# Kernel tuning notes

Measured on AMD Instinct MI355X. Metric: run time of the kernel, lower is better.

The kernel has to match this reference:

```python
import jax, jax.numpy as jnp
import numpy as np

N_NODES = 10000
N_EDGES = 160000
MUL = 16            # multiplicity: emb_dim=64, max_l=1 -> irreps 16x0e + 16x1o
EMB = 64
NUM_BASIS = 10
MAX_RADIUS = 4.5
HIDDEN = 64
N_PATHS = 4         # (0e,0e->0e), (0e,1o->1o), (1o,0e->1o), (1o,1o->0e)
W_NUMEL = N_PATHS * MUL * MUL  # 1024


def setup_inputs() -> dict:
    key = jax.random.key(0)
    ks = jax.random.split(key, 6)
    x = jax.random.normal(ks[0], (N_NODES, EMB), jnp.float32)
    src = jax.random.randint(ks[1], (N_EDGES,), 0, N_NODES)
    dst = jax.random.randint(ks[2], (N_EDGES,), 0, N_NODES)
    edge_vec = jax.random.normal(ks[3], (N_EDGES, 3), jnp.float32)
    mlp_w1 = jax.random.normal(ks[4], (NUM_BASIS, HIDDEN), jnp.float32)
    mlp_w2 = jax.random.normal(ks[5], (HIDDEN, W_NUMEL), jnp.float32)
    return {"x": x, "edge_vec": edge_vec, "mlp_w1": mlp_w1,
            "mlp_w2": mlp_w2, "src": src, "dst": dst}


def _sus(t):
    # e3nn smooth bump helper: exp(-1/t) for t>0 else 0
    return jnp.where(t > 0, jnp.exp(-1.0 / jnp.where(t > 0, t, 1.0)), 0.0)


def _radial_embedding(r):
    # soft_one_hot_linspace(basis='smooth_finite', cutoff=True), then *sqrt(num_basis)
    values = jnp.linspace(0.0, MAX_RADIUS, NUM_BASIS + 2)[1:-1]
    step = MAX_RADIUS / (NUM_BASIS + 1)
    diff = (r[:, None] - values) / step                     # [E, NUM_BASIS]
    basis = 1.14136 * jnp.exp(2.0) * _sus(diff + 1.0) * _sus(1.0 - diff)
    return basis * (NUM_BASIS ** 0.5)


def _forward(x, edge_vec, mlp_w1, mlp_w2, src, dst):
    E = edge_vec.shape[0]
    N = x.shape[0]
    r = jnp.linalg.norm(edge_vec, axis=1)                   # [E]
    # spherical harmonics, lmax=1, normalize=True, 'component' norm: Y0=1, Y1=sqrt(3)*n
    y1 = jnp.sqrt(3.0) * edge_vec / r[:, None]              # [E, 3]

    # radial MLP (e3nn FullyConnectedNet: W~N(0,1), x@W/sqrt(fan_in), relu scaled by sqrt(2))
    emb = _radial_embedding(r)                              # [E, 10]
    h = jnp.sqrt(2.0) * jax.nn.relu(emb @ (mlp_w1 / NUM_BASIS ** 0.5))
    w = h @ (mlp_w2 / HIDDEN ** 0.5)                        # [E, 1024]
    w = w.reshape(E, N_PATHS, MUL, MUL)                     # paths in e3nn order A,B,C,D

    xs = x[src]                                             # gather [E, 64]
    x0 = xs[:, :MUL]                                        # [E, 16] 0e scalars
    x1 = xs[:, MUL:].reshape(E, MUL, 3)                     # [E, 16, 3] 1o vectors

    # Fully connected TP normalization ('component', path_norm 'element'):
    # out0 fan = 2*MUL -> alpha 1/(2*MUL); out1 alpha 3/(2*MUL) with w3j 1/sqrt(3)
    c = 1.0 / jnp.sqrt(2.0 * MUL)
    inv_sqrt3 = 1.0 / jnp.sqrt(3.0)
    wA, wB, wC, wD = w[:, 0], w[:, 1], w[:, 2], w[:, 3]
    # 0e outputs: 0e*0e->0e and 1o*1o->0e (dot product, w3j = I/sqrt(3))
    out0 = c * (jnp.einsum('euw,eu->ew', wA, x0)
                + inv_sqrt3 * jnp.einsum('euw,eum,em->ew', wD, x1, y1))
    # 1o outputs: 0e*1o->1o and 1o*0e->1o (w3j = I/sqrt(3), Y0 = 1)
    out1 = c * (jnp.einsum('euw,eu,em->ewm', wB, x0, y1)
                + jnp.einsum('euw,eum->ewm', wC, x1))
    summand = jnp.concatenate([out0, out1.reshape(E, MUL * 3)], axis=1)  # [E, 64]

    out = jax.ops.segment_sum(summand, dst, num_segments=N)             # [N, 64]
    return out * (N / E)


def reference(x, edge_vec, mlp_w1, mlp_w2, src, dst):
    return _forward(x, edge_vec, mlp_w1, mlp_w2, src, dst)
```

## Files before the change

kernel.cpp:

```cpp
#include <hip/hip_runtime.h>
#include <hip/hip_bf16.h>


typedef __attribute__((ext_vector_type(8))) short bf16x8;
typedef __attribute__((ext_vector_type(4))) float f32x4;

#define NN 10000
#define NE 160000

__device__ __forceinline__ float sus_f(float t) { return t > 0.0f ? __expf(-1.0f / t) : 0.0f; }
__device__ __forceinline__ unsigned int f2bf(float f) {
    unsigned int u = __float_as_uint(f);
    u += 0x7FFFu + ((u >> 16) & 1u);
    return u >> 16;
}
__device__ __forceinline__ float bf2f(unsigned short v) { return __uint_as_float(((unsigned int)v) << 16); }

#define GL16(g, l) __builtin_amdgcn_global_load_lds( \
    (const __attribute__((address_space(1))) void*)(g), \
    (__attribute__((address_space(3))) void*)(l), 16, 0, 0)

__device__ __forceinline__ void stage_lds(const void* g, void* l, int bytes, int wv, int lane) {
    const char* gc = (const char*)g;
    char* lc = (char*)l;
    const int units = bytes >> 4;
    for (int u0 = wv << 6; u0 < units; u0 += 512) {
        if (u0 + lane < units) GL16(gc + (((long)(u0 + lane)) << 4), lc + (u0 << 4));
    }
}

__global__ void hist_k(const int* __restrict__ dst, int* __restrict__ hist,
                       const float* __restrict__ w2, char* __restrict__ w2bf) {
    if (blockIdx.x < 625) {
        const int e = blockIdx.x * 256 + threadIdx.x;
        if (e < NE) atomicAdd(&hist[dst[e]], 1);
    } else {
        const int idx = (blockIdx.x - 625) * 256 + threadIdx.x;
        const int j = idx >> 10, R = idx & 1023;
        unsigned int pk[4];
        #pragma unroll
        for (int p = 0; p < 4; ++p) {
            const unsigned int lo = f2bf(w2[(size_t)(8 * j + 2 * p) * 1024 + R]);
            const unsigned int hi = f2bf(w2[(size_t)(8 * j + 2 * p + 1) * 1024 + R]);
            pk[p] = lo | (hi << 16);
        }
        uint4 v; v.x = pk[0]; v.y = pk[1]; v.z = pk[2]; v.w = pk[3];
        *(uint4*)(w2bf + R * 128 + ((j ^ (R & 7)) << 4)) = v;
    }
}

__global__ __launch_bounds__(1024) void scan_k(const int* __restrict__ hist,
                                               int* __restrict__ offsets) {
    __shared__ int hl[NN];
    __shared__ int wsum[16];
    const int tid = threadIdx.x;
    for (int i = tid; i < NN; i += 1024) hl[i] = hist[i];
    __syncthreads();
    const int base = tid * 10;
    int loc[10]; int s = 0;
    #pragma unroll
    for (int i = 0; i < 10; ++i) { loc[i] = s; const int b = base + i; s += (b < NN) ? hl[b] : 0; }
    int v = s;
    const int lane = tid & 63, wv = tid >> 6;
    #pragma unroll
    for (int d = 1; d < 64; d <<= 1) { int t2 = __shfl_up(v, d); if (lane >= d) v += t2; }
    if (lane == 63) wsum[wv] = v;
    __syncthreads();
    if (tid < 64) {
        int w = (tid < 16) ? wsum[tid] : 0;
        #pragma unroll
        for (int d = 1; d < 16; d <<= 1) { int t2 = __shfl_up(w, d); if (tid >= d) w += t2; }
        if (tid < 16) wsum[tid] = w;
    }
    __syncthreads();
    const int wexc = (wv == 0) ? 0 : wsum[wv - 1];
    const int texc = wexc + v - s;
    #pragma unroll
    for (int i = 0; i < 10; ++i) { const int b = base + i; if (b < NN) offsets[b] = texc + loc[i]; }
    if (tid == 1023) offsets[NN] = texc + s;
}

// ... 12 lines not shown
__global__ __launch_bounds__(256, 4) void prep_k(
    const float* __restrict__ x, const float* __restrict__ edge_vec,
    const float* __restrict__ w1, const int* __restrict__ src,
    const int* __restrict__ perm,
    char* __restrict__ h_bf, char* __restrict__ X0g, char* __restrict__ Zg,
    char* __restrict__ X1g, float* __restrict__ Y1g)
{
    __shared__ float embl[128][10];
    __shared__ float y1l[128][4];
    __shared__ int srcl[128];
    __shared__ float w1l[640];
    const int tid = threadIdx.x;
    const long e0 = (long)blockIdx.x * 128;

    for (int i = tid; i < 640; i += 256) w1l[i] = w1[i];
    if (tid < 128) {
        const int e = tid;
        const int eid = perm[e0 + e];
        const float vx = edge_vec[eid * 3 + 0];
        const float vy = edge_vec[eid * 3 + 1];
        const float vz = edge_vec[eid * 3 + 2];
        const float r = sqrtf(vx * vx + vy * vy + vz * vz);
        const float sc = 1.7320508075688772f / r;
        y1l[e][0] = vx * sc; y1l[e][1] = vy * sc; y1l[e][2] = vz * sc; y1l[e][3] = 0.f;
        *(float4*)&Y1g[(e0 + e) * 4] = make_float4(vx * sc, vy * sc, vz * sc, 0.f);
        srcl[e] = src[eid];
        const float C0 = 1.14136f * __expf(2.0f) * 3.1622776601683795f;
        #pragma unroll
        for (int i = 0; i < 10; ++i) {
            const float diff = r * (11.0f / 4.5f) - (float)(i + 1);
            embl[e][i] = C0 * sus_f(diff + 1.0f) * sus_f(1.0f - diff);
        }
    }
    __syncthreads();
    for (int idx = tid; idx < 1024; idx += 256) {
        const int e = idx >> 3, j = idx & 7;
        float acc[8];
        #pragma unroll
        for (int jj = 0; jj < 8; ++jj) acc[jj] = 0.0f;
        #pragma unroll
        for (int i = 0; i < 10; ++i) {
            const float ei = embl[e][i];
            #pragma unroll
            for (int jj = 0; jj < 8; ++jj) acc[jj] += ei * w1l[i * 64 + j * 8 + jj];
        }
        unsigned int pk[4];
        #pragma unroll
        for (int p = 0; p < 4; ++p) {
            const unsigned int lo = f2bf(fmaxf(acc[2 * p],     0.0f) * 0.4472135954999579f);
            const unsigned int hi = f2bf(fmaxf(acc[2 * p + 1], 0.0f) * 0.4472135954999579f);
            pk[p] = lo | (hi << 16);
        }
        uint4 v; v.x = pk[0]; v.y = pk[1]; v.z = pk[2]; v.w = pk[3];
        *(uint4*)(h_bf + (e0 + e) * 128 + ((j ^ (e & 7)) << 4)) = v;
    }
    for (int idx = tid; idx < 1024; idx += 256) {
        const int e = idx >> 3, p = idx & 7;
        const int s = srcl[e];
        const float2 ab = *(const float2*)&x[(size_t)s * 64 + 2 * p];
        *(unsigned int*)(X0g + (e0 + e) * 36 + p * 4) = f2bf(ab.x) | (f2bf(ab.y) << 16);
    }
    for (int idx = tid; idx < 1024; idx += 256) {
        const int e = idx >> 3, p = idx & 7;
        const int s = srcl[e];
        const float* xp = x + (size_t)s * 64 + 16 + 6 * p;
        const float z0 = xp[0] * y1l[e][0] + xp[1] * y1l[e][1] + xp[2] * y1l[e][2];
        const float z1 = xp[3] * y1l[e][0] + xp[4] * y1l[e][1] + xp[5] * y1l[e][2];
        *(unsigned int*)(Zg + (e0 + e) * 36 + p * 4) = f2bf(z0) | (f2bf(z1) << 16);
    }
    for (int idx = tid; idx < 128 * 12; idx += 256) {
        const int e = idx / 12, qd = idx - e * 12;
        const int s = srcl[e];
        const float4 v = *(const float4*)&x[(size_t)s * 64 + 16 + 4 * qd];
        *(float4*)(X1g + (e0 + e) * 208 + qd * 16) = v;
    }
}

#define BUF_SZ 48128

__global__ __launch_bounds__(512, 2) void se3_edge2(
    const char* __restrict__ w2bf, const char* __restrict__ h_bf,
    const char* __restrict__ X0g, const char* __restrict__ Zg,
    const char* __restrict__ X1g, const float* __restrict__ Y1g,
    const int* __restrict__ dsts, float* __restrict__ out)
{
    __shared__ __align__(16) char w2lds[65536];
    __shared__ __align__(16) char bufs[2][BUF_SZ];
    __shared__ int segst[2][66];
    __shared__ int nseg[2];

    const int tid = threadIdx.x, lane = tid & 63, wv = tid >> 6;
    const int lm = lane & 15, q = lane >> 4;
    const int bx = blockIdx.x;
    const int pair = (bx & 1) ^ ((bx >> 8) & 1);
    const int tb = bx >> 1;
    const int s0 = (q ^ (lm & 7)) << 4;
    const int s1 = s0 ^ 64;
    const int erow = wv << 4;

    const char* w2p0 = w2lds;
    const char* w2p1 = w2lds + 32768;
    {
        const int pa = pair ? 1 : 0, pb = pair ? 2 : 3;
        stage_lds(w2bf + pa * 32768, w2lds, 32768, wv, lane);
        stage_lds(w2bf + pb * 32768, w2lds + 32768, 32768, wv, lane);
        const long e0 = (long)tb * 5 * 128;
        stage_lds(h_bf + e0 * 128, bufs[0], 16384, wv, lane);
        stage_lds(X0g + e0 * 36, bufs[0] + 16384, 4608, wv, lane);
        if (pair) stage_lds(X1g + e0 * 208, bufs[0] + 20992, 26624, wv, lane);
        else      stage_lds(Zg  + e0 * 36,  bufs[0] + 20992, 4608,  wv, lane);
        stage_lds((const char*)(dsts + e0), bufs[0] + 47616, 512, wv, lane);
    }
    __syncthreads();

    const float S = 0.17677669529663687f * 0.125f * 0.0625f;

    for (int tt = 0; tt < 5; ++tt) {
        char* buf = bufs[tt & 1];
        const long gt = (long)tb * 5 + tt;
        const long e0 = gt * 128;
        if (tt < 4) {
            char* nb = bufs[(tt & 1) ^ 1];
            const long ne0 = e0 + 128;
            stage_lds(h_bf + ne0 * 128, nb, 16384, wv, lane);
            stage_lds(X0g + ne0 * 36, nb + 16384, 4608, wv, lane);
            if (pair) stage_lds(X1g + ne0 * 208, nb + 20992, 26624, wv, lane);
            else      stage_lds(Zg  + ne0 * 36,  nb + 20992, 4608,  wv, lane);
            stage_lds((const char*)(dsts + ne0), nb + 47616, 512, wv, lane);
        }
        const char* hl = buf;
        const int arow = erow + lm;
        const bf16x8 a0 = *(const bf16x8*)(hl + arow * 128 + s0);
        const bf16x8 a1 = *(const bf16x8*)(hl + arow * 128 + s1);
        const unsigned short* X0l = (const unsigned short*)(buf + 16384);
        const int* dstl = (const int*)(buf + 47616);

        float ac0[4] = {0,0,0,0}, ac1[4] = {0,0,0,0}, ac2[4] = {0,0,0,0}, ac3[4] = {0,0,0,0};

        if (pair == 0) {
            const unsigned short* Zl = (const unsigned short*)(buf + 20992);
            #pragma unroll 4
            for (int t = 0; t < 16; ++t) {
                const int rowb = (t * 16 + lm) << 7;
                const bf16x8 b00 = *(const bf16x8*)(w2p0 + rowb + s0);
                const bf16x8 b01 = *(const bf16x8*)(w2p0 + rowb + s1);
                const bf16x8 b10 = *(const bf16x8*)(w2p1 + rowb + s0);
                const bf16x8 b11 = *(const bf16x8*)(w2p1 + rowb + s1);
                f32x4 wA = {0.f,0.f,0.f,0.f};
                wA = __builtin_amdgcn_mfma_f32_16x16x32_bf16(a0, b00, wA, 0,0,0);
                wA = __builtin_amdgcn_mfma_f32_16x16x32_bf16(a1, b01, wA, 0,0,0);
                f32x4 wD = {0.f,0.f,0.f,0.f};
                wD = __builtin_amdgcn_mfma_f32_16x16x32_bf16(a0, b10, wD, 0,0,0);
                wD = __builtin_amdgcn_mfma_f32_16x16x32_bf16(a1, b11, wD, 0,0,0);
                #pragma unroll
                for (int r = 0; r < 4; ++r) {
                    const int el = erow + 4 * q + r;
                    ac0[r] += wA[r] * bf2f(X0l[el * 18 + t]);
                    ac1[r] += wD[r] * bf2f(Zl[el * 18 + t]);
                }
            }
            float* summ32 = (float*)buf;
            #pragma unroll
            for (int r = 0; r < 4; ++r) {
                const int el = erow + 4 * q + r;
                summ32[el * 17 + lm] = S * (ac0[r] + 0.5773502691896258f * ac1[r]);
            }
        } else {
            const float* X1l = (const float*)(buf + 20992);
            #pragma unroll 4
            for (int t = 0; t < 16; ++t) {
                const int rowb = (t * 16 + lm) << 7;
                const bf16x8 b00 = *(const bf16x8*)(w2p0 + rowb + s0);
                const bf16x8 b01 = *(const bf16x8*)(w2p0 + rowb + s1);
                const bf16x8 b10 = *(const bf16x8*)(w2p1 + rowb + s0);
                const bf16x8 b11 = *(const bf16x8*)(w2p1 + rowb + s1);
                f32x4 wB = {0.f,0.f,0.f,0.f};
                wB = __builtin_amdgcn_mfma_f32_16x16x32_bf16(a0, b00, wB, 0,0,0);
                wB = __builtin_amdgcn_mfma_f32_16x16x32_bf16(a1, b01, wB, 0,0,0);
                f32x4 wC = {0.f,0.f,0.f,0.f};
                wC = __builtin_amdgcn_mfma_f32_16x16x32_bf16(a0, b10, wC, 0,0,0);
                wC = __builtin_amdgcn_mfma_f32_16x16x32_bf16(a1, b11, wC, 0,0,0);
                #pragma unroll
                for (int r = 0; r < 4; ++r) {
                    const int el = erow + 4 * q + r;
                    ac0[r] += wB[r] * bf2f(X0l[el * 18 + t]);
                    ac1[r] += wC[r] * X1l[el * 52 + 3 * t + 0];
                    ac2[r] += wC[r] * X1l[el * 52 + 3 * t + 1];
                    ac3[r] += wC[r] * X1l[el * 52 + 3 * t + 2];
                }
            }
            unsigned short* summ16 = (unsigned short*)buf;
            #pragma unroll
            for (int r = 0; r < 4; ++r) {
                const int el = erow + 4 * q + r;
                const float4 y = *(const float4*)&Y1g[(e0 + el) * 4];
                const float b = S * ac0[r];
                summ16[el * 49 + 3 * lm + 0] = (unsigned short)f2bf(b * y.x + S * ac1[r]);
                summ16[el * 49 + 3 * lm + 1] = (unsigned short)f2bf(b * y.y + S * ac2[r]);
                summ16[el * 49 + 3 * lm + 2] = (unsigned short)f2bf(b * y.z + S * ac3[r]);
            }
        }
        if (wv < 2) {
            const int base = wv << 6;
            const int d = dstl[base + lane];
            const bool flag = (lane == 0) || (d != dstl[base + lane - 1]);
            const unsigned long long m = __ballot(flag);
            const int sid = (lane == 0) ? 0 : __popcll(m & ((1ull << lane) - 1ull));
            if (flag) segst[wv][sid] = base + lane;
            if (lane == 63) { const int ns = __popcll(m); nseg[wv] = ns; segst[wv][ns] = base + 64; }
        }
        __syncthreads();
        const int nsa = nseg[0], nsb = nseg[1];
        if (pair == 0) {
            const float* summ32 = (const float*)buf;
            const int total = (nsa + nsb) * 16;
            for (int i = tid; i < total; i += 512) {
                const int sg = i >> 4, c = i & 15;
                const int hh = sg >= nsa;
                const int sl = hh ? sg - nsa : sg;
                const int eb = segst[hh][sl], ee = segst[hh][sl + 1];
                float sum = 0.f;
                for (int e = eb; e < ee; ++e) sum += summ32[e * 17 + c];
                atomicAdd(&out[(size_t)dstl[eb] * 64 + c], sum);
            }
        } else {
            const unsigned short* summ16 = (const unsigned short*)buf;
            const int total = (nsa + nsb) * 48;
            for (int i = tid; i < total; i += 512) {
                const int sg = i / 48, c = i - sg * 48;
                const int hh = sg >= nsa;
                const int sl = hh ? sg - nsa : sg;
                const int eb = segst[hh][sl], ee = segst[hh][sl + 1];
                float sum = 0.f;
                for (int e = eb; e < ee; ++e) sum += bf2f(summ16[e * 49 + c]);
                atomicAdd(&out[(size_t)dstl[eb] * 64 + 16 + c], sum);
            }
        }
        __syncthreads();
    }
}

#define FBT 64
template<int PATH>
__device__ __forceinline__ void fb_body(
    const float* __restrict__ x, const float* __restrict__ edge_vec,
    const float* __restrict__ w1, const float* __restrict__ w2,
    const int* __restrict__ src, const int* __restrict__ perm,
    const int* __restrict__ dsts, float* __restrict__ out,
    unsigned short (*w2t)[72], float* arena, float (*y1l)[4],
    int* dstl, int* srcl, int* segstart, int* nseg_s)
{
    constexpr int NC    = (PATH == 0 || PATH == 3) ? 16 : 48;
    constexpr int CBASE = (PATH == 0 || PATH == 3) ? 0 : 16;
    const int tid = threadIdx.x;
    float* embl = arena;
    unsigned short* hl = (unsigned short*)(arena + 640);
    float* feats = arena + 2944;
    float* summ  = arena;
    {
        const float* col = w2 + PATH * 256 + tid;
        #pragma unroll
        for (int k = 0; k < 64; k += 2) {
            const unsigned int lo = f2bf(col[(size_t)k * 1024]);
            const unsigned int hi = f2bf(col[(size_t)(k + 1) * 1024]);
            *(unsigned int*)&w2t[tid][k] = lo | (hi << 16);
        }
    }
    const int lane = tid & 63, wv = tid >> 6, lm = lane & 15, q = lane >> 4;
    const int erow = wv * 16;
    const float C0 = 1.14136f * __expf(2.0f) * 3.1622776601683795f;
    const float S  = 0.17677669529663687f * 0.125f * 0.0625f;
    for (int it = 0; it < 2; ++it) {
        const int e0 = (blockIdx.x * 2 + it) * FBT;
        __syncthreads();
        for (int idx = tid; idx < FBT * 10; idx += 256) {
            const int e = idx / 10, i = idx - e * 10;
            const int eid = perm[e0 + e];
            const float vx = edge_vec[eid * 3 + 0], vy = edge_vec[eid * 3 + 1], vz = edge_vec[eid * 3 + 2];
            const float r = sqrtf(vx * vx + vy * vy + vz * vz);
            const float diff = r * (11.0f / 4.5f) - (float)(i + 1);
            embl[e * 10 + i] = C0 * sus_f(diff + 1.0f) * sus_f(1.0f - diff);
            if (i == 0) {
                const float sc = 1.7320508075688772f / r;
                y1l[e][0] = vx * sc; y1l[e][1] = vy * sc; y1l[e][2] = vz * sc;
                dstl[e] = dsts[e0 + e];
                srcl[e] = src[eid];
            }
        }
        __syncthreads();
// ... 91 lines not shown
            const int eb = segstart[s], ee = segstart[s + 1];
            float sum = 0.0f;
            for (int e = eb; e < ee; ++e) sum += summ[e * NC + c];
            atomicAdd(&out[(size_t)dstl[eb] * 64 + CBASE + c], sum);
        }
    }
}

__global__ __launch_bounds__(256, 2) void fb_edge(
    const float* __restrict__ x, const float* __restrict__ edge_vec,
    const float* __restrict__ w1, const float* __restrict__ w2,
    const int* __restrict__ src, const int* __restrict__ perm,
    const int* __restrict__ dsts, float* __restrict__ out)
{
    __shared__ unsigned short w2t[256][72];
    __shared__ float arena[6016];
    __shared__ float y1l[FBT][4];
    __shared__ int dstl[FBT];
    __shared__ int srcl[FBT];
    __shared__ int segstart[FBT + 1];
    __shared__ int nseg_s;
    switch (blockIdx.y) {
        case 0:  fb_body<0>(x, edge_vec, w1, w2, src, perm, dsts, out, w2t, arena, y1l, dstl, srcl, segstart, &nseg_s); break;
        case 1:  fb_body<1>(x, edge_vec, w1, w2, src, perm, dsts, out, w2t, arena, y1l, dstl, srcl, segstart, &nseg_s); break;
        case 2:  fb_body<2>(x, edge_vec, w1, w2, src, perm, dsts, out, w2t, arena, y1l, dstl, srcl, segstart, &nseg_s); break;
        default: fb_body<3>(x, edge_vec, w1, w2, src, perm, dsts, out, w2t, arena, y1l, dstl, srcl, segstart, &nseg_s); break;
    }
}

extern "C" void kernel_launch(void* const* d_in, const int* in_sizes, int n_in,
                              void* d_out, int out_size, void* d_ws, size_t ws_size,
                              hipStream_t stream) {
    const float* x        = (const float*)d_in[0];
    const float* edge_vec = (const float*)d_in[1];
    const float* w1       = (const float*)d_in[2];
    const float* w2       = (const float*)d_in[3];
    const int*   src      = (const int*)d_in[4];
    const int*   dst      = (const int*)d_in[5];
    float* out = (float*)d_out;

    char* ws = (char*)d_ws;
    size_t off = 0;
    auto alloc = [&](size_t n) -> char* {
        off = (off + 255) & ~(size_t)255;
        char* p = ws + off; off += n; return p;
    };
    int* hist    = (int*)alloc(40000);
    int* cursor  = (int*)alloc(40000);
    int* offsets = (int*)alloc(40004);
    int* perm    = (int*)alloc(640000);
    int* dsts    = (int*)alloc(640000);
    char* w2bf   = alloc(131072);
    char* h_bf   = alloc((size_t)NE * 128);
    char* X0g    = alloc((size_t)NE * 36);
    char* Zg     = alloc((size_t)NE * 36);
    float* Y1g   = (float*)alloc((size_t)NE * 16);
    char* X1g    = alloc((size_t)NE * 208);
    const bool big = (off <= ws_size);

    hipMemsetAsync(d_out, 0, (size_t)out_size * sizeof(float), stream);
    hipMemsetAsync(d_ws, 0, 81408, stream);

    if (big) {
        hipLaunchKernelGGL(hist_k, dim3(657), dim3(256), 0, stream, dst, hist, w2, w2bf);
        hipLaunchKernelGGL(scan_k, dim3(1), dim3(1024), 0, stream, hist, offsets);
        hipLaunchKernelGGL(scatter_k, dim3(625), dim3(256), 0, stream, dst, offsets, cursor, perm, dsts);
        hipLaunchKernelGGL(prep_k, dim3(1250), dim3(256), 0, stream,
                           x, edge_vec, w1, src, perm, h_bf, X0g, Zg, X1g, Y1g);
        hipLaunchKernelGGL(se3_edge2, dim3(500), dim3(512), 0, stream,
                           w2bf, h_bf, X0g, Zg, X1g, Y1g, dsts, out);
    } else {
        hipLaunchKernelGGL(hist_k, dim3(625), dim3(256), 0, stream, dst, hist, w2, w2bf);
        hipLaunchKernelGGL(scan_k, dim3(1), dim3(1024), 0, stream, hist, offsets);
        hipLaunchKernelGGL(scatter_k, dim3(625), dim3(256), 0, stream, dst, offsets, cursor, perm, dsts);
        hipLaunchKernelGGL(fb_edge, dim3(1250, 4), dim3(256), 0, stream,
                           x, edge_vec, w1, w2, src, perm, dsts, out);
    }
}
```

Measured before the change: 126.8 us.

## Split edge kernel into per-path kernels with smaller LDS footprint

Replaces the single paired-path edge kernel, which kept two w2 slices in LDS, with two kernels (A/D and B/C). Each block stages only one 32KB w2 slice, so more blocks can share a CU. The A operand h is now read directly from global instead of being staged, X1 is packed as bf16 in a transposed per-tile layout, and the per-edge features are held in registers. The cost is reading h_bf twice per edge pair, an extra launch, and a further bf16 rounding of X1.

```diff
diff --git a/kernel.cpp b/kernel.cpp
--- a/kernel.cpp
+++ b/kernel.cpp
@@ -3,6 +3,7 @@
 
 
 typedef __attribute__((ext_vector_type(8))) short bf16x8;
+typedef __attribute__((ext_vector_type(8))) unsigned short u16x8;
 typedef __attribute__((ext_vector_type(4))) float f32x4;
 
 #define NN 10000
@@ -15,18 +16,19 @@
     return u >> 16;
 }
 __device__ __forceinline__ float bf2f(unsigned short v) { return __uint_as_float(((unsigned int)v) << 16); }
+__device__ __forceinline__ float bflo(unsigned int v) { return __uint_as_float(v << 16); }
+__device__ __forceinline__ float bfhi(unsigned int v) { return __uint_as_float(v & 0xFFFF0000u); }
+__device__ __forceinline__ float bfe(u16x8 v, int i) { return __uint_as_float(((unsigned int)v[i]) << 16); }
 
 #define GL16(g, l) __builtin_amdgcn_global_load_lds( \
     (const __attribute__((address_space(1))) void*)(g), \
     (__attribute__((address_space(3))) void*)(l), 16, 0, 0)
 
-__device__ __forceinline__ void stage_lds(const void* g, void* l, int bytes, int wv, int lane) {
+__device__ __forceinline__ void stageN(const void* g, void* l, int bytes, int tid, int nthr) {
     const char* gc = (const char*)g;
     char* lc = (char*)l;
     const int units = bytes >> 4;
-    for (int u0 = wv << 6; u0 < units; u0 += 512) {
-        if (u0 + lane < units) GL16(gc + (((long)(u0 + lane)) << 4), lc + (u0 << 4));
-    }
+    for (int u = tid; u < units; u += nthr) GL16(gc + ((long)u << 4), lc + (u << 4));
 }
 
 __global__ void hist_k(const int* __restrict__ dst, int* __restrict__ hist,
@@ -145,13 +147,13 @@
             pk[p] = lo | (hi << 16);
         }
         uint4 v; v.x = pk[0]; v.y = pk[1]; v.z = pk[2]; v.w = pk[3];
-        *(uint4*)(h_bf + (e0 + e) * 128 + ((j ^ (e & 7)) << 4)) = v;
+        *(uint4*)(h_bf + (e0 + e) * 128 + (j << 4)) = v;
     }
     for (int idx = tid; idx < 1024; idx += 256) {
         const int e = idx >> 3, p = idx & 7;
         const int s = srcl[e];
         const float2 ab = *(const float2*)&x[(size_t)s * 64 + 2 * p];
-        *(unsigned int*)(X0g + (e0 + e) * 36 + p * 4) = f2bf(ab.x) | (f2bf(ab.y) << 16);
+        *(unsigned int*)(X0g + (e0 + e) * 32 + p * 4) = f2bf(ab.x) | (f2bf(ab.y) << 16);
     }
     for (int idx = tid; idx < 1024; idx += 256) {
         const int e = idx >> 3, p = idx & 7;
@@ -159,139 +161,83 @@
         const float* xp = x + (size_t)s * 64 + 16 + 6 * p;
         const float z0 = xp[0] * y1l[e][0] + xp[1] * y1l[e][1] + xp[2] * y1l[e][2];
         const float z1 = xp[3] * y1l[e][0] + xp[4] * y1l[e][1] + xp[5] * y1l[e][2];
-        *(unsigned int*)(Zg + (e0 + e) * 36 + p * 4) = f2bf(z0) | (f2bf(z1) << 16);
-    }
-    for (int idx = tid; idx < 128 * 12; idx += 256) {
-        const int e = idx / 12, qd = idx - e * 12;
+        *(unsigned int*)(Zg + (e0 + e) * 32 + p * 4) = f2bf(z0) | (f2bf(z1) << 16);
+    }
+    for (int idx = tid; idx < 2048; idx += 256) {
+        const int e = idx >> 4, u = idx & 15;
         const int s = srcl[e];
-        const float4 v = *(const float4*)&x[(size_t)s * 64 + 16 + 4 * qd];
-        *(float4*)(X1g + (e0 + e) * 208 + qd * 16) = v;
-    }
-}
-
-#define BUF_SZ 48128
-
-__global__ __launch_bounds__(512, 2) void se3_edge2(
+        const float* xp = x + (size_t)s * 64 + 16 + 3 * u;
+        uint2 v;
+        v.x = f2bf(xp[0]) | (f2bf(xp[1]) << 16);
+        v.y = f2bf(xp[2]);
+        *(uint2*)(X1g + (size_t)blockIdx.x * 16384 + ((u << 7) + e) * 8) = v;
+    }
+}
+
+__global__ __launch_bounds__(512, 6) void edge_ad(
     const char* __restrict__ w2bf, const char* __restrict__ h_bf,
     const char* __restrict__ X0g, const char* __restrict__ Zg,
-    const char* __restrict__ X1g, const float* __restrict__ Y1g,
     const int* __restrict__ dsts, float* __restrict__ out)
 {
-    __shared__ __align__(16) char w2lds[65536];
-    __shared__ __align__(16) char bufs[2][BUF_SZ];
+    __shared__ __align__(16) char w2lds[32768];
+    __shared__ __align__(16) char feats[2][4608];
+    __shared__ float summ[16 * 132];
     __shared__ int segst[2][66];
     __shared__ int nseg[2];
 
     const int tid = threadIdx.x, lane = tid & 63, wv = tid >> 6;
-    const int lm = lane & 15, q = lane >> 4;
-    const int bx = blockIdx.x;
-    const int pair = (bx & 1) ^ ((bx >> 8) & 1);
-    const int tb = bx >> 1;
-    const int s0 = (q ^ (lm & 7)) << 4;
-    const int s1 = s0 ^ 64;
-    const int erow = wv << 4;
-
-    const char* w2p0 = w2lds;
-    const char* w2p1 = w2lds + 32768;
+    const int lm = lane & 15, q = lane >> 4, erow = wv << 4;
+    const int isD = blockIdx.y;
+    const char* featg = isD ? Zg : X0g;
+    const int tb = blockIdx.x;
+    const int s0 = (q ^ (lm & 7)) << 4, s1 = s0 ^ 64;
+    const float S = 0.17677669529663687f * 0.125f * 0.0625f;
+    const float scl = isD ? S * 0.5773502691896258f : S;
+
+    stageN(w2bf + (isD ? 3 : 0) * 32768, w2lds, 32768, tid, 512);
     {
-        const int pa = pair ? 1 : 0, pb = pair ? 2 : 3;
-        stage_lds(w2bf + pa * 32768, w2lds, 32768, wv, lane);
-        stage_lds(w2bf + pb * 32768, w2lds + 32768, 32768, wv, lane);
         const long e0 = (long)tb * 5 * 128;
-        stage_lds(h_bf + e0 * 128, bufs[0], 16384, wv, lane);
-        stage_lds(X0g + e0 * 36, bufs[0] + 16384, 4608, wv, lane);
-        if (pair) stage_lds(X1g + e0 * 208, bufs[0] + 20992, 26624, wv, lane);
-        else      stage_lds(Zg  + e0 * 36,  bufs[0] + 20992, 4608,  wv, lane);
-        stage_lds((const char*)(dsts + e0), bufs[0] + 47616, 512, wv, lane);
+        stageN(featg + e0 * 32, feats[0], 4096, tid, 512);
+        stageN((const char*)(dsts + e0), feats[0] + 4096, 512, tid, 512);
     }
     __syncthreads();
 
-    const float S = 0.17677669529663687f * 0.125f * 0.0625f;
-
     for (int tt = 0; tt < 5; ++tt) {
-        char* buf = bufs[tt & 1];
-        const long gt = (long)tb * 5 + tt;
-        const long e0 = gt * 128;
+        char* fb = feats[tt & 1];
+        const long e0 = ((long)tb * 5 + tt) * 128;
         if (tt < 4) {
-            char* nb = bufs[(tt & 1) ^ 1];
-            const long ne0 = e0 + 128;
-            stage_lds(h_bf + ne0 * 128, nb, 16384, wv, lane);
-            stage_lds(X0g + ne0 * 36, nb + 16384, 4608, wv, lane);
-            if (pair) stage_lds(X1g + ne0 * 208, nb + 20992, 26624, wv, lane);
-            else      stage_lds(Zg  + ne0 * 36,  nb + 20992, 4608,  wv, lane);
-            stage_lds((const char*)(dsts + ne0), nb + 47616, 512, wv, lane);
-        }
-        const char* hl = buf;
+            char* nb = feats[(tt & 1) ^ 1];
+            stageN(featg + (e0 + 128) * 32, nb, 4096, tid, 512);
+            stageN((const char*)(dsts + e0 + 128), nb + 4096, 512, tid, 512);
+        }
         const int arow = erow + lm;
-        const bf16x8 a0 = *(const bf16x8*)(hl + arow * 128 + s0);
-        const bf16x8 a1 = *(const bf16x8*)(hl + arow * 128 + s1);
-        const unsigned short* X0l = (const unsigned short*)(buf + 16384);
-        const int* dstl = (const int*)(buf + 47616);
-
-        float ac0[4] = {0,0,0,0}, ac1[4] = {0,0,0,0}, ac2[4] = {0,0,0,0}, ac3[4] = {0,0,0,0};
-
-        if (pair == 0) {
-            const unsigned short* Zl = (const unsigned short*)(buf + 20992);
-            #pragma unroll 4
-            for (int t = 0; t < 16; ++t) {
-                const int rowb = (t * 16 + lm) << 7;
-                const bf16x8 b00 = *(const bf16x8*)(w2p0 + rowb + s0);
-                const bf16x8 b01 = *(const bf16x8*)(w2p0 + rowb + s1);
-                const bf16x8 b10 = *(const bf16x8*)(w2p1 + rowb + s0);
-                const bf16x8 b11 = *(const bf16x8*)(w2p1 + rowb + s1);
-                f32x4 wA = {0.f,0.f,0.f,0.f};
-                wA = __builtin_amdgcn_mfma_f32_16x16x32_bf16(a0, b00, wA, 0,0,0);
-                wA = __builtin_amdgcn_mfma_f32_16x16x32_bf16(a1, b01, wA, 0,0,0);
-                f32x4 wD = {0.f,0.f,0.f,0.f};
-                wD = __builtin_amdgcn_mfma_f32_16x16x32_bf16(a0, b10, wD, 0,0,0);
-                wD = __builtin_amdgcn_mfma_f32_16x16x32_bf16(a1, b11, wD, 0,0,0);
-                #pragma unroll
-                for (int r = 0; r < 4; ++r) {
-                    const int el = erow + 4 * q + r;
-                    ac0[r] += wA[r] * bf2f(X0l[el * 18 + t]);
-                    ac1[r] += wD[r] * bf2f(Zl[el * 18 + t]);
-                }
-            }
-            float* summ32 = (float*)buf;
-            #pragma unroll
-            for (int r = 0; r < 4; ++r) {
-                const int el = erow + 4 * q + r;
-                summ32[el * 17 + lm] = S * (ac0[r] + 0.5773502691896258f * ac1[r]);
-            }
-        } else {
-            const float* X1l = (const float*)(buf + 20992);
-            #pragma unroll 4
-            for (int t = 0; t < 16; ++t) {
-                const int rowb = (t * 16 + lm) << 7;
-                const bf16x8 b00 = *(const bf16x8*)(w2p0 + rowb + s0);
-                const bf16x8 b01 = *(const bf16x8*)(w2p0 + rowb + s1);
-                const bf16x8 b10 = *(const bf16x8*)(w2p1 + rowb + s0);
-                const bf16x8 b11 = *(const bf16x8*)(w2p1 + rowb + s1);
-                f32x4 wB = {0.f,0.f,0.f,0.f};
-                wB = __builtin_amdgcn_mfma_f32_16x16x32_bf16(a0, b00, wB, 0,0,0);
-                wB = __builtin_amdgcn_mfma_f32_16x16x32_bf16(a1, b01, wB, 0,0,0);
-                f32x4 wC = {0.f,0.f,0.f,0.f};
-                wC = __builtin_amdgcn_mfma_f32_16x16x32_bf16(a0, b10, wC, 0,0,0);
-                wC = __builtin_amdgcn_mfma_f32_16x16x32_bf16(a1, b11, wC, 0,0,0);
-                #pragma unroll
-                for (int r = 0; r < 4; ++r) {
-                    const int el = erow + 4 * q + r;
-                    ac0[r] += wB[r] * bf2f(X0l[el * 18 + t]);
-                    ac1[r] += wC[r] * X1l[el * 52 + 3 * t + 0];
-                    ac2[r] += wC[r] * X1l[el * 52 + 3 * t + 1];
-                    ac3[r] += wC[r] * X1l[el * 52 + 3 * t + 2];
-                }
-            }
-            unsigned short* summ16 = (unsigned short*)buf;
-            #pragma unroll
-            for (int r = 0; r < 4; ++r) {
-                const int el = erow + 4 * q + r;
-                const float4 y = *(const float4*)&Y1g[(e0 + el) * 4];
-                const float b = S * ac0[r];
-                summ16[el * 49 + 3 * lm + 0] = (unsigned short)f2bf(b * y.x + S * ac1[r]);
-                summ16[el * 49 + 3 * lm + 1] = (unsigned short)f2bf(b * y.y + S * ac2[r]);
-                summ16[el * 49 + 3 * lm + 2] = (unsigned short)f2bf(b * y.z + S * ac3[r]);
-            }
+        const bf16x8 a0 = *(const bf16x8*)(h_bf + (e0 + arow) * 128 + q * 16);
+        const bf16x8 a1 = *(const bf16x8*)(h_bf + (e0 + arow) * 128 + 64 + q * 16);
+        u16x8 flo[4], fhi[4];
+        #pragma unroll
+        for (int r = 0; r < 4; ++r) {
+            const int el = erow + 4 * q + r;
+            flo[r] = *(const u16x8*)(fb + el * 32);
+            fhi[r] = *(const u16x8*)(fb + el * 32 + 16);
+        }
+        float ac[4] = {0.f, 0.f, 0.f, 0.f};
+        #pragma unroll
+        for (int t = 0; t < 16; ++t) {
+            const int rowb = (t * 16 + lm) << 7;
+            const bf16x8 b0 = *(const bf16x8*)(w2lds + rowb + s0);
+            const bf16x8 b1 = *(const bf16x8*)(w2lds + rowb + s1);
+            f32x4 w = {0.f, 0.f, 0.f, 0.f};
+            w = __builtin_amdgcn_mfma_f32_16x16x32_bf16(a0, b0, w, 0, 0, 0);
+            w = __builtin_amdgcn_mfma_f32_16x16x32_bf16(a1, b1, w, 0, 0, 0);
+            #pragma unroll
+            for (int r = 0; r < 4; ++r)
+                ac[r] += w[r] * (t < 8 ? bfe(flo[r], t) : bfe(fhi[r], t - 8));
+        }
+        const int* dstl = (const int*)(fb + 4096);
+        #pragma unroll
+        for (int r = 0; r < 4; ++r) {
+            const int el = erow + 4 * q + r;
+            summ[lm * 132 + el] = scl * ac[r];
         }
         if (wv < 2) {
             const int base = wv << 6;
@@ -304,30 +250,143 @@
         }
         __syncthreads();
         const int nsa = nseg[0], nsb = nseg[1];
-        if (pair == 0) {
-            const float* summ32 = (const float*)buf;
-            const int total = (nsa + nsb) * 16;
-            for (int i = tid; i < total; i += 512) {
-                const int sg = i >> 4, c = i & 15;
-                const int hh = sg >= nsa;
-                const int sl = hh ? sg - nsa : sg;
-                const int eb = segst[hh][sl], ee = segst[hh][sl + 1];
-                float sum = 0.f;
-                for (int e = eb; e < ee; ++e) sum += summ32[e * 17 + c];
-                atomicAdd(&out[(size_t)dstl[eb] * 64 + c], sum);
-            }
+        const int total = (nsa + nsb) << 4;
+        for (int i = tid; i < total; i += 512) {
+            const int sg = i >> 4, c = i & 15;
+            const int hh = (sg >= nsa) ? 1 : 0;
+            const int sl = hh ? sg - nsa : sg;
+            const int eb = segst[hh][sl], ee = segst[hh][sl + 1];
+            float s = 0.f;
+            for (int e = eb; e < ee; ++e) s += summ[c * 132 + e];
+            atomicAdd(&out[(size_t)dstl[eb] * 64 + c], s);
+        }
+        __syncthreads();
+    }
+}
+
+#define FEATSZ 16896
+
+__global__ __launch_bounds__(512, 4) void edge_bc(
+    const char* __restrict__ w2bf, const char* __restrict__ h_bf,
+    const char* __restrict__ X0g, const char* __restrict__ X1g,
+    const float* __restrict__ Y1g, const int* __restrict__ dsts,
+    float* __restrict__ out)
+{
+    __shared__ __align__(16) char w2lds[32768];
+    __shared__ __align__(16) char feats[2][FEATSZ];
+    __shared__ unsigned short summ[48 * 132];
+    __shared__ int segst[2][66];
+    __shared__ int nseg[2];
+
+    const int tid = threadIdx.x, lane = tid & 63, wv = tid >> 6;
+    const int lm = lane & 15, q = lane >> 4, erow = wv << 4;
+    const int isC = blockIdx.y;
+    const int tb = blockIdx.x;
+    const int s0 = (q ^ (lm & 7)) << 4, s1 = s0 ^ 64;
+    const int dstoff = isC ? 16384 : 6144;
+    const float S = 0.17677669529663687f * 0.125f * 0.0625f;
+
+    auto stage_tile = [&](char* nb, long e0) {
+        if (isC) {
+            stageN(X1g + (e0 >> 7) * 16384, nb, 16384, tid, 512);
         } else {
-            const unsigned short* summ16 = (const unsigned short*)buf;
-            const int total = (nsa + nsb) * 48;
-            for (int i = tid; i < total; i += 512) {
-                const int sg = i / 48, c = i - sg * 48;
-                const int hh = sg >= nsa;
-                const int sl = hh ? sg - nsa : sg;
-                const int eb = segst[hh][sl], ee = segst[hh][sl + 1];
-                float sum = 0.f;
-                for (int e = eb; e < ee; ++e) sum += bf2f(summ16[e * 49 + c]);
-                atomicAdd(&out[(size_t)dstl[eb] * 64 + 16 + c], sum);
-            }
+            stageN(X0g + e0 * 32, nb, 4096, tid, 512);
+            stageN((const char*)(Y1g + e0 * 4), nb + 4096, 2048, tid, 512);
+        }
+        stageN((const char*)(dsts + e0), nb + dstoff, 512, tid, 512);
+    };
+
+    stageN(w2bf + (isC ? 2 : 1) * 32768, w2lds, 32768, tid, 512);
+    stage_tile(feats[0], (long)tb * 5 * 128);
+    __syncthreads();
+
+    for (int tt = 0; tt < 5; ++tt) {
+        char* fb = feats[tt & 1];
+        const long e0 = ((long)tb * 5 + tt) * 128;
+        if (tt < 4) stage_tile(feats[(tt & 1) ^ 1], e0 + 128);
+
+        const int arow = erow + lm;
+        const bf16x8 a0 = *(const bf16x8*)(h_bf + (e0 + arow) * 128 + q * 16);
+        const bf16x8 a1 = *(const bf16x8*)(h_bf + (e0 + arow) * 128 + 64 + q * 16);
+
+        if (isC) {
+            float ac1[4] = {0,0,0,0}, ac2[4] = {0,0,0,0}, ac3[4] = {0,0,0,0};
+            #pragma unroll
+            for (int t = 0; t < 16; ++t) {
+                const int rowb = (t * 16 + lm) << 7;
+                const bf16x8 b0 = *(const bf16x8*)(w2lds + rowb + s0);
+                const bf16x8 b1 = *(const bf16x8*)(w2lds + rowb + s1);
+                f32x4 w = {0.f, 0.f, 0.f, 0.f};
+                w = __builtin_amdgcn_mfma_f32_16x16x32_bf16(a0, b0, w, 0, 0, 0);
+                w = __builtin_amdgcn_mfma_f32_16x16x32_bf16(a1, b1, w, 0, 0, 0);
+                #pragma unroll
+                for (int r = 0; r < 4; ++r) {
+                    const int el = erow + 4 * q + r;
+                    const uint2 xv = *(const uint2*)(fb + ((t << 7) + el) * 8);
+                    ac1[r] += w[r] * bflo(xv.x);
+                    ac2[r] += w[r] * bfhi(xv.x);
+                    ac3[r] += w[r] * bflo(xv.y);
+                }
+            }
+            #pragma unroll
+            for (int r = 0; r < 4; ++r) {
+                const int el = erow + 4 * q + r;
+                summ[(3 * lm + 0) * 132 + el] = (unsigned short)f2bf(S * ac1[r]);
+                summ[(3 * lm + 1) * 132 + el] = (unsigned short)f2bf(S * ac2[r]);
+                summ[(3 * lm + 2) * 132 + el] = (unsigned short)f2bf(S * ac3[r]);
+            }
+        } else {
+            u16x8 flo[4], fhi[4];
+            #pragma unroll
+            for (int r = 0; r < 4; ++r) {
+                const int el = erow + 4 * q + r;
+                flo[r] = *(const u16x8*)(fb + el * 32);
+                fhi[r] = *(const u16x8*)(fb + el * 32 + 16);
+            }
+            float ac[4] = {0.f, 0.f, 0.f, 0.f};
+            #pragma unroll
+            for (int t = 0; t < 16; ++t) {
+                const int rowb = (t * 16 + lm) << 7;
+                const bf16x8 b0 = *(const bf16x8*)(w2lds + rowb + s0);
+                const bf16x8 b1 = *(const bf16x8*)(w2lds + rowb + s1);
+                f32x4 w = {0.f, 0.f, 0.f, 0.f};
+                w = __builtin_amdgcn_mfma_f32_16x16x32_bf16(a0, b0, w, 0, 0, 0);
+                w = __builtin_amdgcn_mfma_f32_16x16x32_bf16(a1, b1, w, 0, 0, 0);
+                #pragma unroll
+                for (int r = 0; r < 4; ++r)
+                    ac[r] += w[r] * (t < 8 ? bfe(flo[r], t) : bfe(fhi[r], t - 8));
+            }
+            #pragma unroll
+            for (int r = 0; r < 4; ++r) {
+                const int el = erow + 4 * q + r;
+                const float4 y = *(const float4*)(fb + 4096 + el * 16);
+                const float b = S * ac[r];
+                summ[(3 * lm + 0) * 132 + el] = (unsigned short)f2bf(b * y.x);
+                summ[(3 * lm + 1) * 132 + el] = (unsigned short)f2bf(b * y.y);
+                summ[(3 * lm + 2) * 132 + el] = (unsigned short)f2bf(b * y.z);
+            }
+        }
+        const int* dstl = (const int*)(fb + dstoff);
+        if (wv < 2) {
+            const int base = wv << 6;
+            const int d = dstl[base + lane];
+            const bool flag = (lane == 0) || (d != dstl[base + lane - 1]);
+            const unsigned long long m = __ballot(flag);
+            const int sid = (lane == 0) ? 0 : __popcll(m & ((1ull << lane) - 1ull));
+            if (flag) segst[wv][sid] = base + lane;
+            if (lane == 63) { const int ns = __popcll(m); nseg[wv] = ns; segst[wv][ns] = base + 64; }
+        }
+        __syncthreads();
+        const int nsa = nseg[0], nsb = nseg[1];
+        const int total = (nsa + nsb) * 48;
+        for (int i = tid; i < total; i += 512) {
+            const int sg = i / 48, c = i - sg * 48;
+            const int hh = (sg >= nsa) ? 1 : 0;
+            const int sl = hh ? sg - nsa : sg;
+            const int eb = segst[hh][sl], ee = segst[hh][sl + 1];
+            float s = 0.f;
+            for (int e = eb; e < ee; ++e) s += bf2f(summ[c * 132 + e]);
+            atomicAdd(&out[(size_t)dstl[eb] * 64 + 16 + c], s);
         }
         __syncthreads();
     }
@@ -525,10 +584,10 @@
     int* dsts    = (int*)alloc(640000);
     char* w2bf   = alloc(131072);
     char* h_bf   = alloc((size_t)NE * 128);
-    char* X0g    = alloc((size_t)NE * 36);
-    char* Zg     = alloc((size_t)NE * 36);
+    char* X0g    = alloc((size_t)NE * 32);
+    char* Zg     = alloc((size_t)NE * 32);
+    char* X1g    = alloc((size_t)NE * 128);
     float* Y1g   = (float*)alloc((size_t)NE * 16);
-    char* X1g    = alloc((size_t)NE * 208);
     const bool big = (off <= ws_size);
 
     hipMemsetAsync(d_out, 0, (size_t)out_size * sizeof(float), stream);
@@ -540,8 +599,10 @@
         hipLaunchKernelGGL(scatter_k, dim3(625), dim3(256), 0, stream, dst, offsets, cursor, perm, dsts);
         hipLaunchKernelGGL(prep_k, dim3(1250), dim3(256), 0, stream,
                            x, edge_vec, w1, src, perm, h_bf, X0g, Zg, X1g, Y1g);
-        hipLaunchKernelGGL(se3_edge2, dim3(500), dim3(512), 0, stream,
-                           w2bf, h_bf, X0g, Zg, X1g, Y1g, dsts, out);
+        hipLaunchKernelGGL(edge_bc, dim3(250, 2), dim3(512), 0, stream,
+                           w2bf, h_bf, X0g, X1g, Y1g, dsts, out);
+        hipLaunchKernelGGL(edge_ad, dim3(250, 2), dim3(512), 0, stream,
+                           w2bf, h_bf, X0g, Zg, dsts, out);
     } else {
         hipLaunchKernelGGL(hist_k, dim3(625), dim3(256), 0, stream, dst, hist, w2, w2bf);
         hipLaunchKernelGGL(scan_k, dim3(1), dim3(1024), 0, stream, hist, offsets);
```

Measured after the change: 153.8 us. 1.21x slower.

## Compact per-edge staging layouts, load hidden activations directly, separate summand buffer

Applied to the files above, without the earlier changes.

Prep now stores X0/Z at 32 bytes per edge instead of 36, and stores X1 as bf16 in a component-major tile layout. Y1 is staged into LDS rather than read from global memory. The edge kernel reads the MLP hidden activations straight from global memory into MFMA operands instead of staging them through LDS. It also preloads the X0/Z values into registers, writes summands to a dedicated transposed LDS buffer, and launches a 2D grid by path pair. The aim is to cut global and LDS traffic and the per-buffer LDS footprint. In exchange X1 loses precision from fp32 to bf16, and the unstaged h loads may add latency.

```diff
diff --git a/kernel.cpp b/kernel.cpp
--- a/kernel.cpp
+++ b/kernel.cpp
@@ -3,6 +3,7 @@
 
 
 typedef __attribute__((ext_vector_type(8))) short bf16x8;
+typedef __attribute__((ext_vector_type(8))) unsigned short u16x8;
 typedef __attribute__((ext_vector_type(4))) float f32x4;
 
 #define NN 10000
@@ -15,18 +16,19 @@
     return u >> 16;
 }
 __device__ __forceinline__ float bf2f(unsigned short v) { return __uint_as_float(((unsigned int)v) << 16); }
+__device__ __forceinline__ float bflo(unsigned int v) { return __uint_as_float(v << 16); }
+__device__ __forceinline__ float bfhi(unsigned int v) { return __uint_as_float(v & 0xFFFF0000u); }
+__device__ __forceinline__ float bfe(u16x8 v, int i) { return __uint_as_float(((unsigned int)v[i]) << 16); }
 
 #define GL16(g, l) __builtin_amdgcn_global_load_lds( \
     (const __attribute__((address_space(1))) void*)(g), \
     (__attribute__((address_space(3))) void*)(l), 16, 0, 0)
 
-__device__ __forceinline__ void stage_lds(const void* g, void* l, int bytes, int wv, int lane) {
+__device__ __forceinline__ void stageN(const void* g, void* l, int bytes, int tid, int nthr) {
     const char* gc = (const char*)g;
     char* lc = (char*)l;
     const int units = bytes >> 4;
-    for (int u0 = wv << 6; u0 < units; u0 += 512) {
-        if (u0 + lane < units) GL16(gc + (((long)(u0 + lane)) << 4), lc + (u0 << 4));
-    }
+    for (int u = tid; u < units; u += nthr) GL16(gc + ((long)u << 4), lc + (u << 4));
 }
 
 __global__ void hist_k(const int* __restrict__ dst, int* __restrict__ hist,
@@ -145,13 +147,13 @@
             pk[p] = lo | (hi << 16);
         }
         uint4 v; v.x = pk[0]; v.y = pk[1]; v.z = pk[2]; v.w = pk[3];
-        *(uint4*)(h_bf + (e0 + e) * 128 + ((j ^ (e & 7)) << 4)) = v;
+        *(uint4*)(h_bf + (e0 + e) * 128 + (j << 4)) = v;
     }
     for (int idx = tid; idx < 1024; idx += 256) {
         const int e = idx >> 3, p = idx & 7;
         const int s = srcl[e];
         const float2 ab = *(const float2*)&x[(size_t)s * 64 + 2 * p];
-        *(unsigned int*)(X0g + (e0 + e) * 36 + p * 4) = f2bf(ab.x) | (f2bf(ab.y) << 16);
+        *(unsigned int*)(X0g + (e0 + e) * 32 + p * 4) = f2bf(ab.x) | (f2bf(ab.y) << 16);
     }
     for (int idx = tid; idx < 1024; idx += 256) {
         const int e = idx >> 3, p = idx & 7;
@@ -159,140 +161,150 @@
         const float* xp = x + (size_t)s * 64 + 16 + 6 * p;
         const float z0 = xp[0] * y1l[e][0] + xp[1] * y1l[e][1] + xp[2] * y1l[e][2];
         const float z1 = xp[3] * y1l[e][0] + xp[4] * y1l[e][1] + xp[5] * y1l[e][2];
-        *(unsigned int*)(Zg + (e0 + e) * 36 + p * 4) = f2bf(z0) | (f2bf(z1) << 16);
-    }
-    for (int idx = tid; idx < 128 * 12; idx += 256) {
-        const int e = idx / 12, qd = idx - e * 12;
+        *(unsigned int*)(Zg + (e0 + e) * 32 + p * 4) = f2bf(z0) | (f2bf(z1) << 16);
+    }
+    for (int idx = tid; idx < 2048; idx += 256) {
+        const int e = idx >> 4, u = idx & 15;
         const int s = srcl[e];
-        const float4 v = *(const float4*)&x[(size_t)s * 64 + 16 + 4 * qd];
-        *(float4*)(X1g + (e0 + e) * 208 + qd * 16) = v;
-    }
-}
-
-#define BUF_SZ 48128
-
-__global__ __launch_bounds__(512, 2) void se3_edge2(
+        const float* xp = x + (size_t)s * 64 + 16 + 3 * u;
+        uint2 v;
+        v.x = f2bf(xp[0]) | (f2bf(xp[1]) << 16);
+        v.y = f2bf(xp[2]);
+        *(uint2*)(X1g + (size_t)blockIdx.x * 16384 + ((u << 7) + e) * 8) = v;
+    }
+}
+
+#define DSTOFF 22784
+#define EBUF 23296
+
+__global__ __launch_bounds__(512, 2) void se3_edge(
     const char* __restrict__ w2bf, const char* __restrict__ h_bf,
     const char* __restrict__ X0g, const char* __restrict__ Zg,
     const char* __restrict__ X1g, const float* __restrict__ Y1g,
     const int* __restrict__ dsts, float* __restrict__ out)
 {
     __shared__ __align__(16) char w2lds[65536];
-    __shared__ __align__(16) char bufs[2][BUF_SZ];
+    __shared__ __align__(16) char bufs[2][EBUF];
+    __shared__ __align__(16) char summb[12672];
     __shared__ int segst[2][66];
     __shared__ int nseg[2];
 
     const int tid = threadIdx.x, lane = tid & 63, wv = tid >> 6;
-    const int lm = lane & 15, q = lane >> 4;
-    const int bx = blockIdx.x;
-    const int pair = (bx & 1) ^ ((bx >> 8) & 1);
-    const int tb = bx >> 1;
-    const int s0 = (q ^ (lm & 7)) << 4;
-    const int s1 = s0 ^ 64;
-    const int erow = wv << 4;
+    const int lm = lane & 15, q = lane >> 4, erow = wv << 4;
+    const int pair = blockIdx.y;
+    const int tb = blockIdx.x;
+    const int s0 = (q ^ (lm & 7)) << 4, s1 = s0 ^ 64;
+    const float S = 0.17677669529663687f * 0.125f * 0.0625f;
+
+    auto stage_tile = [&](char* nb, long e0) {
+        stageN(X0g + e0 * 32, nb, 4096, tid, 512);
+        if (pair == 0) {
+            stageN(Zg + e0 * 32, nb + 4096, 4096, tid, 512);
+        } else {
+            stageN(X1g + (e0 >> 7) * 16384, nb + 4096, 16384, tid, 512);
+            stageN((const char*)(Y1g + e0 * 4), nb + 20736, 2048, tid, 512);
+        }
+        stageN((const char*)(dsts + e0), nb + DSTOFF, 512, tid, 512);
+    };
 
     const char* w2p0 = w2lds;
     const char* w2p1 = w2lds + 32768;
+    const long e00 = (long)tb * 5 * 128;
     {
         const int pa = pair ? 1 : 0, pb = pair ? 2 : 3;
-        stage_lds(w2bf + pa * 32768, w2lds, 32768, wv, lane);
-        stage_lds(w2bf + pb * 32768, w2lds + 32768, 32768, wv, lane);
-        const long e0 = (long)tb * 5 * 128;
-        stage_lds(h_bf + e0 * 128, bufs[0], 16384, wv, lane);
-        stage_lds(X0g + e0 * 36, bufs[0] + 16384, 4608, wv, lane);
-        if (pair) stage_lds(X1g + e0 * 208, bufs[0] + 20992, 26624, wv, lane);
-        else      stage_lds(Zg  + e0 * 36,  bufs[0] + 20992, 4608,  wv, lane);
-        stage_lds((const char*)(dsts + e0), bufs[0] + 47616, 512, wv, lane);
+        stageN(w2bf + pa * 32768, w2lds, 32768, tid, 512);
+        stageN(w2bf + pb * 32768, w2lds + 32768, 32768, tid, 512);
+        stage_tile(bufs[0], e00);
     }
     __syncthreads();
 
-    const float S = 0.17677669529663687f * 0.125f * 0.0625f;
+    const int arow = erow + lm;
 
     for (int tt = 0; tt < 5; ++tt) {
-        char* buf = bufs[tt & 1];
-        const long gt = (long)tb * 5 + tt;
-        const long e0 = gt * 128;
-        if (tt < 4) {
-            char* nb = bufs[(tt & 1) ^ 1];
-            const long ne0 = e0 + 128;
-            stage_lds(h_bf + ne0 * 128, nb, 16384, wv, lane);
-            stage_lds(X0g + ne0 * 36, nb + 16384, 4608, wv, lane);
-            if (pair) stage_lds(X1g + ne0 * 208, nb + 20992, 26624, wv, lane);
-            else      stage_lds(Zg  + ne0 * 36,  nb + 20992, 4608,  wv, lane);
-            stage_lds((const char*)(dsts + ne0), nb + 47616, 512, wv, lane);
-        }
-        const char* hl = buf;
-        const int arow = erow + lm;
-        const bf16x8 a0 = *(const bf16x8*)(hl + arow * 128 + s0);
-        const bf16x8 a1 = *(const bf16x8*)(hl + arow * 128 + s1);
-        const unsigned short* X0l = (const unsigned short*)(buf + 16384);
-        const int* dstl = (const int*)(buf + 47616);
+        char* fb = bufs[tt & 1];
+        const long e0 = e00 + (long)tt * 128;
+        if (tt < 4) stage_tile(bufs[(tt & 1) ^ 1], e0 + 128);
+
+        const bf16x8 a0 = *(const bf16x8*)(h_bf + (e0 + arow) * 128 + q * 16);
+        const bf16x8 a1 = *(const bf16x8*)(h_bf + (e0 + arow) * 128 + 64 + q * 16);
+
+        u16x8 flo[4], fhi[4];
+        #pragma unroll
+        for (int r = 0; r < 4; ++r) {
+            const int el = erow + 4 * q + r;
+            flo[r] = *(const u16x8*)(fb + el * 32);
+            fhi[r] = *(const u16x8*)(fb + el * 32 + 16);
+        }
 
         float ac0[4] = {0,0,0,0}, ac1[4] = {0,0,0,0}, ac2[4] = {0,0,0,0}, ac3[4] = {0,0,0,0};
 
         if (pair == 0) {
-            const unsigned short* Zl = (const unsigned short*)(buf + 20992);
-            #pragma unroll 4
+            u16x8 zlo[4], zhi[4];
+            #pragma unroll
+            for (int r = 0; r < 4; ++r) {
+                const int el = erow + 4 * q + r;
+                zlo[r] = *(const u16x8*)(fb + 4096 + el * 32);
+                zhi[r] = *(const u16x8*)(fb + 4096 + el * 32 + 16);
+            }
+            #pragma unroll
             for (int t = 0; t < 16; ++t) {
                 const int rowb = (t * 16 + lm) << 7;
                 const bf16x8 b00 = *(const bf16x8*)(w2p0 + rowb + s0);
                 const bf16x8 b01 = *(const bf16x8*)(w2p0 + rowb + s1);
                 const bf16x8 b10 = *(const bf16x8*)(w2p1 + rowb + s0);
                 const bf16x8 b11 = *(const bf16x8*)(w2p1 + rowb + s1);
-                f32x4 wA = {0.f,0.f,0.f,0.f};
+                f32x4 wA = {0.f,0.f,0.f,0.f}, wD = {0.f,0.f,0.f,0.f};
                 wA = __builtin_amdgcn_mfma_f32_16x16x32_bf16(a0, b00, wA, 0,0,0);
                 wA = __builtin_amdgcn_mfma_f32_16x16x32_bf16(a1, b01, wA, 0,0,0);
-                f32x4 wD = {0.f,0.f,0.f,0.f};
                 wD = __builtin_amdgcn_mfma_f32_16x16x32_bf16(a0, b10, wD, 0,0,0);
                 wD = __builtin_amdgcn_mfma_f32_16x16x32_bf16(a1, b11, wD, 0,0,0);
                 #pragma unroll
                 for (int r = 0; r < 4; ++r) {
-                    const int el = erow + 4 * q + r;
-                    ac0[r] += wA[r] * bf2f(X0l[el * 18 + t]);
-                    ac1[r] += wD[r] * bf2f(Zl[el * 18 + t]);
+                    ac0[r] += wA[r] * (t < 8 ? bfe(flo[r], t) : bfe(fhi[r], t - 8));
+                    ac1[r] += wD[r] * (t < 8 ? bfe(zlo[r], t) : bfe(zhi[r], t - 8));
                 }
             }
-            float* summ32 = (float*)buf;
+            float* summ32 = (float*)summb;
             #pragma unroll
             for (int r = 0; r < 4; ++r) {
                 const int el = erow + 4 * q + r;
-                summ32[el * 17 + lm] = S * (ac0[r] + 0.5773502691896258f * ac1[r]);
+                summ32[lm * 132 + el] = S * (ac0[r] + 0.5773502691896258f * ac1[r]);
             }
         } else {
-            const float* X1l = (const float*)(buf + 20992);
-            #pragma unroll 4
+            #pragma unroll
             for (int t = 0; t < 16; ++t) {
                 const int rowb = (t * 16 + lm) << 7;
                 const bf16x8 b00 = *(const bf16x8*)(w2p0 + rowb + s0);
                 const bf16x8 b01 = *(const bf16x8*)(w2p0 + rowb + s1);
                 const bf16x8 b10 = *(const bf16x8*)(w2p1 + rowb + s0);
                 const bf16x8 b11 = *(const bf16x8*)(w2p1 + rowb + s1);
-                f32x4 wB = {0.f,0.f,0.f,0.f};
+                f32x4 wB = {0.f,0.f,0.f,0.f}, wC = {0.f,0.f,0.f,0.f};
                 wB = __builtin_amdgcn_mfma_f32_16x16x32_bf16(a0, b00, wB, 0,0,0);
                 wB = __builtin_amdgcn_mfma_f32_16x16x32_bf16(a1, b01, wB, 0,0,0);
-                f32x4 wC = {0.f,0.f,0.f,0.f};
                 wC = __builtin_amdgcn_mfma_f32_16x16x32_bf16(a0, b10, wC, 0,0,0);
                 wC = __builtin_amdgcn_mfma_f32_16x16x32_bf16(a1, b11, wC, 0,0,0);
                 #pragma unroll
                 for (int r = 0; r < 4; ++r) {
                     const int el = erow + 4 * q + r;
-                    ac0[r] += wB[r] * bf2f(X0l[el * 18 + t]);
-                    ac1[r] += wC[r] * X1l[el * 52 + 3 * t + 0];
-                    ac2[r] += wC[r] * X1l[el * 52 + 3 * t + 1];
-                    ac3[r] += wC[r] * X1l[el * 52 + 3 * t + 2];
+                    const uint2 xv = *(const uint2*)(fb + 4096 + ((t << 7) + el) * 8);
+                    ac0[r] += wB[r] * (t < 8 ? bfe(flo[r], t) : bfe(fhi[r], t - 8));
+                    ac1[r] += wC[r] * bflo(xv.x);
+                    ac2[r] += wC[r] * bfhi(xv.x);
+                    ac3[r] += wC[r] * bflo(xv.y);
                 }
             }
-            unsigned short* summ16 = (unsigned short*)buf;
+            unsigned short* summ16 = (unsigned short*)summb;
             #pragma unroll
             for (int r = 0; r < 4; ++r) {
                 const int el = erow + 4 * q + r;
-                const float4 y = *(const float4*)&Y1g[(e0 + el) * 4];
+                const float4 y = *(const float4*)(fb + 20736 + el * 16);
                 const float b = S * ac0[r];
-                summ16[el * 49 + 3 * lm + 0] = (unsigned short)f2bf(b * y.x + S * ac1[r]);
-                summ16[el * 49 + 3 * lm + 1] = (unsigned short)f2bf(b * y.y + S * ac2[r]);
-                summ16[el * 49 + 3 * lm + 2] = (unsigned short)f2bf(b * y.z + S * ac3[r]);
-            }
-        }
+                summ16[(3 * lm + 0) * 132 + el] = (unsigned short)f2bf(b * y.x + S * ac1[r]);
+                summ16[(3 * lm + 1) * 132 + el] = (unsigned short)f2bf(b * y.y + S * ac2[r]);
+                summ16[(3 * lm + 2) * 132 + el] = (unsigned short)f2bf(b * y.z + S * ac3[r]);
+            }
+        }
+        const int* dstl = (const int*)(fb + DSTOFF);
         if (wv < 2) {
             const int base = wv << 6;
             const int d = dstl[base + lane];
@@ -305,28 +317,28 @@
         __syncthreads();
         const int nsa = nseg[0], nsb = nseg[1];
         if (pair == 0) {
-            const float* summ32 = (const float*)buf;
-            const int total = (nsa + nsb) * 16;
+            const float* sm = (const float*)summb;
+            const int total = (nsa + nsb) << 4;
             for (int i = tid; i < total; i += 512) {
                 const int sg = i >> 4, c = i & 15;
-                const int hh = sg >= nsa;
+                const int hh = (sg >= nsa) ? 1 : 0;
                 const int sl = hh ? sg - nsa : sg;
                 const int eb = segst[hh][sl], ee = segst[hh][sl + 1];
-                float sum = 0.f;
-                for (int e = eb; e < ee; ++e) sum += summ32[e * 17 + c];
-                atomicAdd(&out[(size_t)dstl[eb] * 64 + c], sum);
+                float s = 0.f;
+                for (int e = eb; e < ee; ++e) s += sm[c * 132 + e];
+                atomicAdd(&out[(size_t)dstl[eb] * 64 + c], s);
             }
         } else {
-            const unsigned short* summ16 = (const unsigned short*)buf;
+            const unsigned short* sm = (const unsigned short*)summb;
             const int total = (nsa + nsb) * 48;
             for (int i = tid; i < total; i += 512) {
                 const int sg = i / 48, c = i - sg * 48;
-                const int hh = sg >= nsa;
+                const int hh = (sg >= nsa) ? 1 : 0;
                 const int sl = hh ? sg - nsa : sg;
                 const int eb = segst[hh][sl], ee = segst[hh][sl + 1];
-                float sum = 0.f;
-                for (int e = eb; e < ee; ++e) sum += bf2f(summ16[e * 49 + c]);
-                atomicAdd(&out[(size_t)dstl[eb] * 64 + 16 + c], sum);
+                float s = 0.f;
+                for (int e = eb; e < ee; ++e) s += bf2f(sm[c * 132 + e]);
+                atomicAdd(&out[(size_t)dstl[eb] * 64 + 16 + c], s);
             }
         }
         __syncthreads();
@@ -525,10 +537,10 @@
     int* dsts    = (int*)alloc(640000);
     char* w2bf   = alloc(131072);
     char* h_bf   = alloc((size_t)NE * 128);
-    char* X0g    = alloc((size_t)NE * 36);
-    char* Zg     = alloc((size_t)NE * 36);
+    char* X0g    = alloc((size_t)NE * 32);
+    char* Zg     = alloc((size_t)NE * 32);
+    char* X1g    = alloc((size_t)NE * 128);
     float* Y1g   = (float*)alloc((size_t)NE * 16);
-    char* X1g    = alloc((size_t)NE * 208);
     const bool big = (off <= ws_size);
 
     hipMemsetAsync(d_out, 0, (size_t)out_size * sizeof(float), stream);
@@ -540,7 +552,7 @@
         hipLaunchKernelGGL(scatter_k, dim3(625), dim3(256), 0, stream, dst, offsets, cursor, perm, dsts);
         hipLaunchKernelGGL(prep_k, dim3(1250), dim3(256), 0, stream,
                            x, edge_vec, w1, src, perm, h_bf, X0g, Zg, X1g, Y1g);
-        hipLaunchKernelGGL(se3_edge2, dim3(500), dim3(512), 0, stream,
+        hipLaunchKernelGGL(se3_edge, dim3(250, 2), dim3(512), 0, stream,
                            w2bf, h_bf, X0g, Zg, X1g, Y1g, dsts, out);
     } else {
         hipLaunchKernelGGL(hist_k, dim3(625), dim3(256), 0, stream, dst, hist, w2, w2bf);
```

After: 127.5 us. About the same (+0.5%).
